# Performance work log

Hardware: AMD Instinct MI355X
Metric: run time of the kernel (lower is better)

## Reference

```python
import jax, jax.numpy as jnp
import numpy as np
import math

N_EMBD = 512
N_BRANCH = 4
BLOCK = 2048
B, T = 2, 2048


def make_rope_tables(dim, max_len):
    inv_freq = 1.0 / (10000.0 ** (np.arange(0, dim, 2, dtype=np.float32) / dim))
    t = np.arange(max_len, dtype=np.float32)
    freqs = np.einsum('i,j->ij', t, inv_freq)  # [max_len, dim/2]
    return jnp.asarray(np.cos(freqs)), jnp.asarray(np.sin(freqs))


def apply_rope(xq, cos, sin):
    # xq: [..., T, C]; cos/sin: [T, C/2]
    x1 = xq[..., 0::2]
    x2 = xq[..., 1::2]
    y1 = x1 * cos - x2 * sin
    y2 = x1 * sin + x2 * cos
    return jnp.stack((y1, y2), axis=-1).reshape(xq.shape)


def setup_inputs() -> dict:
    key = jax.random.key(0)
    ks = jax.random.split(key, 6)
    C, NB = N_EMBD, N_BRANCH
    s = 1.0 / math.sqrt(C)
    a = jax.random.normal(ks[0], (B, T, C), jnp.float32)
    x = jax.random.normal(ks[1], (B, T, C), jnp.float32)
    Wq = jax.random.normal(ks[2], (C, C * NB), jnp.float32) * s
    Wk = jax.random.normal(ks[3], (C, C), jnp.float32) * s
    Wv = jax.random.normal(ks[4], (C, C * NB), jnp.float32) * s
    Wo = jax.random.normal(ks[5], (C, C), jnp.float32) * s
    cos, sin = make_rope_tables(C, BLOCK)
    return {"a": a, "x": x, "Wq": Wq, "Wk": Wk, "Wv": Wv, "Wo": Wo,
            "cos": cos, "sin": sin}


def reference(a, x, Wq, Wk, Wv, Wo, cos, sin):
    Bb, Tt, C = x.shape
    NB = Wq.shape[1] // C
    cos_t = cos[:Tt]
    sin_t = sin[:Tt]

    q = (a @ Wq).reshape(Bb, Tt, NB, C).transpose(0, 2, 1, 3)  # [B,NB,T,C]
    v = (a @ Wv).reshape(Bb, Tt, NB, C).transpose(0, 2, 1, 3)  # [B,NB,T,C]
    k = (x @ Wk)[:, None, :, :]                                # [B,1,T,C]

    q = apply_rope(q, cos_t, sin_t)
    k = apply_rope(k, cos_t, sin_t)

    att = jnp.einsum('bntc,bosc->bnts', q, k) / math.sqrt(C)   # [B,NB,T,T]
    causal = jnp.tril(jnp.ones((Tt, Tt), bool))                # [T,T]
    att_m = jnp.where(causal, att, -jnp.inf)

    # softmax over branch axis; mask is identical across branches, so compute
    # on unmasked logits and zero-out masked positions (== nan_to_num of
    # softmax over fully -inf columns)
    soft_probs = jnp.where(causal, jax.nn.softmax(att, axis=1), 0.0)

    max_val = jnp.max(soft_probs, axis=1, keepdims=True)
    hard_mask = jax.lax.stop_gradient((soft_probs == max_val).astype(att.dtype))
    route_mask = jax.lax.stop_gradient(hard_mask - soft_probs) + soft_probs

    att_max = jnp.max(att_m, axis=1)                           # [B,T,T]
    attn_probs = jax.nn.softmax(att_max, axis=-1)              # [B,T,T]

    combined = attn_probs[:, None, :, :] * route_mask          # [B,NB,T,T]
    y = jnp.einsum('bnts,bnsc->btc', combined, v)              # [B,T,C]
    return y @ Wo
```

## Files before the change

kernel.cpp:

```cpp
#include <hip/hip_runtime.h>
#include <math.h>


#define B_ 2
#define T_ 2048
#define C_ 512
#define NB_ 4
#define C2_ 1024

typedef unsigned short u16;
typedef unsigned char u8;
using short8 = __attribute__((ext_vector_type(8))) short;
using bf16x8 = __attribute__((ext_vector_type(8))) __bf16;
using f32x4  = __attribute__((ext_vector_type(4))) float;

__device__ __forceinline__ float bf2f(u16 u) {
  union { unsigned int i; float f; } v; v.i = ((unsigned int)u) << 16; return v.f;
}
__device__ __forceinline__ u16 f2bf(float f) {
  union { float f; unsigned int i; } v; v.f = f;
  unsigned int u = v.i;
  return (u16)((u + 0x7fffu + ((u >> 16) & 1u)) >> 16);
}
__device__ __forceinline__ f32x4 mfma16x16x32(short8 a, short8 b, f32x4 c) {
  return __builtin_amdgcn_mfma_f32_16x16x32_bf16(
      __builtin_bit_cast(bf16x8, a), __builtin_bit_cast(bf16x8, b), c, 0, 0, 0);
}
__device__ __forceinline__ void split8(const float* s, uint4& hi, uint4& lo) {
  u16 h[8], l[8];
#pragma unroll
  for (int j = 0; j < 8; ++j) {
    h[j] = f2bf(s[j]);
    l[j] = f2bf(s[j] - bf2f(h[j]));
  }
  hi.x = h[0] | ((unsigned)h[1] << 16); hi.y = h[2] | ((unsigned)h[3] << 16);
  hi.z = h[4] | ((unsigned)h[5] << 16); hi.w = h[6] | ((unsigned)h[7] << 16);
  lo.x = l[0] | ((unsigned)l[1] << 16); lo.y = l[2] | ((unsigned)l[3] << 16);
  lo.z = l[4] | ((unsigned)l[5] << 16); lo.w = l[6] | ((unsigned)l[7] << 16);
}
__device__ __forceinline__ int swz(int row) { return ((row >> 1) & 3) << 3; }

template <int MODE>
__global__ __launch_bounds__(256) void gemm_qk(const float* __restrict__ A,
                                               const float* __restrict__ W,
                                               u16* __restrict__ out,
                                               const float* __restrict__ cosT,
                                               const float* __restrict__ sinT,
                                               const int N, const int K) {
  __shared__ u16 Ah[64][32], Al[64][32];
  __shared__ u16 Bh[64][32], Bl[64][32];
  const int tid = threadIdx.x;
  const int wave = tid >> 6, lane = tid & 63;
  const int m0 = blockIdx.y << 6, n0 = blockIdx.x << 6;
  const f32x4 zero = {0.f, 0.f, 0.f, 0.f};
  f32x4 acc[4] = {zero, zero, zero, zero};
  const int srow = tid >> 2, koff = ((tid & 3) << 3) ^ swz(tid >> 2);
  const int lrow = lane & 15, lk = ((lane >> 4) << 3) ^ swz(lane & 15);
  for (int kk = 0; kk < K; kk += 32) {
    const int kg = (tid & 3) << 3;
    float av[8];
    *(float4*)(av) = *(const float4*)(&A[(size_t)(m0 + srow) * K + kk + kg]);
    *(float4*)(av + 4) =
        *(const float4*)(&A[(size_t)(m0 + srow) * K + kk + kg + 4]);
    uint4 hi, lo;
    split8(av, hi, lo);
    *(uint4*)(&Ah[srow][koff]) = hi;
    *(uint4*)(&Al[srow][koff]) = lo;
    float wv[8];
#pragma unroll
    for (int j = 0; j < 8; ++j)
      wv[j] = W[(size_t)(kk + kg + j) * N + n0 + srow];
    split8(wv, hi, lo);
    *(uint4*)(&Bh[srow][koff]) = hi;
    *(uint4*)(&Bl[srow][koff]) = lo;
    __syncthreads();
    short8 ah = *(const short8*)(&Ah[(wave << 4) + lrow][lk]);
    short8 al = *(const short8*)(&Al[(wave << 4) + lrow][lk]);
#pragma unroll
    for (int ns = 0; ns < 4; ++ns) {
      short8 bh = *(const short8*)(&Bh[(ns << 4) + lrow][lk]);
      short8 bl = *(const short8*)(&Bl[(ns << 4) + lrow][lk]);
      acc[ns] = mfma16x16x32(ah, bh, acc[ns]);
      acc[ns] = mfma16x16x32(al, bh, acc[ns]);
      acc[ns] = mfma16x16x32(ah, bl, acc[ns]);
    }
    __syncthreads();
  }
  const int r0 = m0 + (wave << 4) + ((lane >> 4) << 2);
  const int cb = n0 + (lane & 15);
#pragma unroll
  for (int ns = 0; ns < 4; ++ns) {
#pragma unroll
    for (int r = 0; r < 4; ++r) {
      const int rg = r0 + r;
      const int cg = cb + (ns << 4);
      float v = acc[ns][r];
      float pv = __shfl_xor(v, 1);
      const int t = rg & (T_ - 1);
      const int c = (MODE == 1) ? (cg & (C_ - 1)) : cg;
      const int i = c >> 1;
      const float cf = cosT[(t << 8) + i];
      const float sf = sinT[(t << 8) + i];
      float x1 = (lane & 1) ? pv : v;
      float x2 = (lane & 1) ? v : pv;
      float y = (lane & 1) ? (x1 * sf + x2 * cf) : (x1 * cf - x2 * sf);
      if (MODE == 1) y *= 0.044194173824159216f;
      const u16 hi = f2bf(y);
      const u16 lo = f2bf(y - bf2f(hi));
      size_t rowoff;
      if (MODE == 1) {
        const int b = rg >> 11, n = cg >> 9;
        rowoff = ((size_t)((b * NB_ + n) * T_ + t)) * C2_;
      } else {
        rowoff = (size_t)rg * C2_;
      }
      out[rowoff + c] = hi;
      out[rowoff + C_ + c] = lo;
    }
  }
}

template <int AF32, int OF32>
__global__ __launch_bounds__(256) void gemm_hi(const void* __restrict__ Ap,
                                               const float* __restrict__ W,
                                               void* __restrict__ outp,
                                               const int N, const int K) {
  __shared__ u16 As[64][32];
  __shared__ u16 Bs[64][32];
  const int tid = threadIdx.x;
  const int wave = tid >> 6, lane = tid & 63;
  const int m0 = blockIdx.y << 6, n0 = blockIdx.x << 6;
  const f32x4 zero = {0.f, 0.f, 0.f, 0.f};
  f32x4 acc[4] = {zero, zero, zero, zero};
  const int srow = tid >> 2, koff = ((tid & 3) << 3) ^ swz(tid >> 2);
  const int lrow = lane & 15, lk = ((lane >> 4) << 3) ^ swz(lane & 15);
  for (int kk = 0; kk < K; kk += 32) {
    const int kg = (tid & 3) << 3;
    if (AF32) {
      const float* A = (const float*)Ap;
      float av[8];
      *(float4*)(av) = *(const float4*)(&A[(size_t)(m0 + srow) * K + kk + kg]);
      *(float4*)(av + 4) =
          *(const float4*)(&A[(size_t)(m0 + srow) * K + kk + kg + 4]);
      uint4 hi;
      hi.x = f2bf(av[0]) | ((unsigned)f2bf(av[1]) << 16);
      hi.y = f2bf(av[2]) | ((unsigned)f2bf(av[3]) << 16);
      hi.z = f2bf(av[4]) | ((unsigned)f2bf(av[5]) << 16);
      hi.w = f2bf(av[6]) | ((unsigned)f2bf(av[7]) << 16);
      *(uint4*)(&As[srow][koff]) = hi;
    } else {
      const u16* A = (const u16*)Ap;
      *(uint4*)(&As[srow][koff]) =
          *(const uint4*)(&A[(size_t)(m0 + srow) * K + kk + kg]);
    }
    uint4 hi;
    {
      float w[8];
#pragma unroll
      for (int j = 0; j < 8; ++j)
        w[j] = W[(size_t)(kk + kg + j) * N + n0 + srow];
      hi.x = f2bf(w[0]) | ((unsigned)f2bf(w[1]) << 16);
      hi.y = f2bf(w[2]) | ((unsigned)f2bf(w[3]) << 16);
      hi.z = f2bf(w[4]) | ((unsigned)f2bf(w[5]) << 16);
      hi.w = f2bf(w[6]) | ((unsigned)f2bf(w[7]) << 16);
    }
    *(uint4*)(&Bs[srow][koff]) = hi;
    __syncthreads();
    short8 af = *(const short8*)(&As[(wave << 4) + lrow][lk]);
#pragma unroll
    for (int ns = 0; ns < 4; ++ns) {
      short8 bf = *(const short8*)(&Bs[(ns << 4) + lrow][lk]);
      acc[ns] = mfma16x16x32(af, bf, acc[ns]);
    }
    __syncthreads();
  }
  const int r0 = m0 + (wave << 4) + ((lane >> 4) << 2);
  const int cb = n0 + (lane & 15);
#pragma unroll
  for (int ns = 0; ns < 4; ++ns) {
#pragma unroll
    for (int r = 0; r < 4; ++r) {
      const size_t idx = (size_t)(r0 + r) * N + cb + (ns << 4);
      if (OF32) ((float*)outp)[idx] = acc[ns][r];
      else ((u16*)outp)[idx] = f2bf(acc[ns][r]);
    }
  }
}

__global__ __launch_bounds__(256) void transpose_v_k(const u16* __restrict__ Vraw,
                                                     u16* __restrict__ VT) {
  const int bid = blockIdx.x;
  const int ct = bid & 7;
  const int ttile = (bid >> 3) & 31;
  const int n = (bid >> 8) & 3;
  const int b = bid >> 10;
  __shared__ u16 tile[64][68];
  const int tid = threadIdx.x;
  const int rr = tid >> 4;
  const int cc = (tid & 15) << 2;
  const int t0 = ttile << 6, c0 = ct << 6;
#pragma unroll
  for (int it = 0; it < 4; ++it) {
    const int r = (it << 4) + rr;
    *(ushort4*)(&tile[r][cc]) = *(const ushort4*)(
        &Vraw[((size_t)((b << 11) + t0 + r)) * (NB_ * C_) + n * C_ + c0 + cc]);
  }
  __syncthreads();
#pragma unroll
  for (int it = 0; it < 4; ++it) {
    const int c = (it << 4) + rr;
    ushort4 w;
    w.x = tile[cc + 0][c]; w.y = tile[cc + 1][c];
    w.z = tile[cc + 2][c]; w.w = tile[cc + 3][c];
    *(ushort4*)(&VT[((size_t)((b * NB_ + n) * C_ + c0 + c)) * T_ + t0 + cc]) = w;
  }
}

__global__ __launch_bounds__(256) void scores_k(const u16* __restrict__ Qcat,
                                                const u16* __restrict__ Kcat,
                                                u16* __restrict__ Mout,
                                                u8* __restrict__ Mask) {
  const int tri = ((blockIdx.x & 7) * 66) + (blockIdx.x >> 3);
  int tt = (int)((sqrtf(8.f * (float)tri + 1.f) - 1.f) * 0.5f);
  while ((tt + 1) * (tt + 2) / 2 <= tri) ++tt;
  while (tt * (tt + 1) / 2 > tri) --tt;
  const int ss = tri - tt * (tt + 1) / 2;
  const int b = blockIdx.y;
  __shared__ __align__(16) u16 Qh[NB_][64][32], Ql[NB_][64][32];
  __shared__ __align__(16) u16 Kh[64][32], Kl[64][32];
  const int tid = threadIdx.x;
  const int wave = tid >> 6, lane = tid & 63;
  const int t0 = tt << 6, s0 = ss << 6;
  const f32x4 zero = {0.f, 0.f, 0.f, 0.f};
  f32x4 acc[NB_][4];
  for (int n = 0; n < NB_; ++n)
    for (int j = 0; j < 4; ++j) acc[n][j] = zero;
  const int srow = tid >> 2, kg = (tid & 3) << 3;
  const int lrow = lane & 15, lk = (lane >> 4) << 3;
  const int wrow = wave << 4;
  const size_t qstride = (size_t)T_ * C2_;
  const size_t qbase = ((size_t)(b * NB_ * T_ + t0 + srow)) * C2_ + kg;
  const size_t kbase = ((size_t)((b << 11) + s0 + srow)) * C2_ + kg;

  for (int kk = 0; kk < C_; kk += 32) {
#pragma unroll
    for (int n = 0; n < NB_; ++n) {
      const size_t qb = qbase + (size_t)n * qstride + kk;
      __builtin_amdgcn_global_load_lds(
          (const __attribute__((address_space(1))) void*)&Qcat[qb],
          (__attribute__((address_space(3))) void*)&Qh[n][wrow][0], 16, 0, 0);
      __builtin_amdgcn_global_load_lds(
          (const __attribute__((address_space(1))) void*)&Qcat[qb + C_],
          (__attribute__((address_space(3))) void*)&Ql[n][wrow][0], 16, 0, 0);
    }
    __builtin_amdgcn_global_load_lds(
        (const __attribute__((address_space(1))) void*)&Kcat[kbase + kk],
        (__attribute__((address_space(3))) void*)&Kh[wrow][0], 16, 0, 0);
    __builtin_amdgcn_global_load_lds(
        (const __attribute__((address_space(1))) void*)&Kcat[kbase + kk + C_],
        (__attribute__((address_space(3))) void*)&Kl[wrow][0], 16, 0, 0);
    __syncthreads();
    short8 qh[NB_], ql[NB_];
#pragma unroll
    for (int n = 0; n < NB_; ++n) {
      qh[n] = *(const short8*)(&Qh[n][wrow + lrow][lk]);
      ql[n] = *(const short8*)(&Ql[n][wrow + lrow][lk]);
    }
#pragma unroll
    for (int ns = 0; ns < 4; ++ns) {
      short8 kh = *(const short8*)(&Kh[(ns << 4) + lrow][lk]);
      short8 kl = *(const short8*)(&Kl[(ns << 4) + lrow][lk]);
#pragma unroll
      for (int n = 0; n < NB_; ++n) {
        acc[n][ns] = mfma16x16x32(qh[n], kh, acc[n][ns]);
        acc[n][ns] = mfma16x16x32(ql[n], kh, acc[n][ns]);
        acc[n][ns] = mfma16x16x32(qh[n], kl, acc[n][ns]);
      }
    }
    __syncthreads();
  }
  const int tb = t0 + (wave << 4) + ((lane >> 4) << 2);
  const int sb = s0 + (lane & 15);
#pragma unroll
  for (int ns = 0; ns < 4; ++ns) {
#pragma unroll
    for (int r = 0; r < 4; ++r) {
      const int t = tb + r, s = sb + (ns << 4);
      float a0 = acc[0][ns][r], a1 = acc[1][ns][r];
      float a2 = acc[2][ns][r], a3 = acc[3][ns][r];
      float m = fmaxf(fmaxf(a0, a1), fmaxf(a2, a3));
      u8 msk = (u8)((a0 == m) | ((a1 == m) << 1) | ((a2 == m) << 2) |
                    ((a3 == m) << 3));
      if (s > t) { m = -__builtin_inff(); msk = 0; }
      const size_t idx = (size_t)b * T_ * T_ + (size_t)t * T_ + s;
      Mout[idx] = f2bf(m);
      Mask[idx] = msk;
    }
  }
}

__global__ __launch_bounds__(256) void rowstats_k(const u16* __restrict__ Mb,
                                                  float* __restrict__ Rm,
                                                  float* __restrict__ Rz) {
  const int r = (blockIdx.x << 2) + (threadIdx.x >> 6);
  const int lane = threadIdx.x & 63;
  const int b = r >> 11, t = r & (T_ - 1);
  const u16* row = Mb + (size_t)b * T_ * T_ + (size_t)t * T_;
  float m = -__builtin_inff();
  for (int s = lane; s <= t; s += 64) m = fmaxf(m, bf2f(row[s]));
#pragma unroll
  for (int off = 32; off; off >>= 1) m = fmaxf(m, __shfl_xor(m, off));
  float z = 0.f;
  for (int s = lane; s <= t; s += 64) z += __expf(bf2f(row[s]) - m);
#pragma unroll
  for (int off = 32; off; off >>= 1) z += __shfl_xor(z, off);
  if (lane == 0) { Rm[r] = m; Rz[r] = 1.f / z; }
}

__global__ __launch_bounds__(512) void pv_k(const u16* __restrict__ Mb,
                                            const float* __restrict__ Rm,
                                            const float* __restrict__ Rz,
                                            const u8* __restrict__ Mask,
                                            const u16* __restrict__ VT,
                                            u16* __restrict__ Y) {
  const int cblk = blockIdx.x, ypair = blockIdx.y, b = blockIdx.z;
  const int c0 = cblk << 6;
  __shared__ u16 Ps[NB_][64][32];
  __shared__ u16 Vs[NB_][64][32];
  const int tid = threadIdx.x;
  const int wave = tid >> 6, lane = tid & 63;
  const int wq = wave & 3, ch = wave >> 2;
  const int row8 = tid >> 3, off4 = (tid & 7) << 2;
  const int scol = off4 ^ swz(row8);
  const int lrow = lane & 15, lk = ((lane >> 4) << 3) ^ swz(lane & 15);
  const f32x4 zero = {0.f, 0.f, 0.f, 0.f};
  const size_t vrow_base[NB_] = {
      ((size_t)((b * NB_ + 0) * C_ + c0 + row8)) * T_,
      ((size_t)((b * NB_ + 1) * C_ + c0 + row8)) * T_,
      ((size_t)((b * NB_ + 2) * C_ + c0 + row8)) * T_,
      ((size_t)((b * NB_ + 3) * C_ + c0 + row8)) * T_};

  for (int half = 0; half < 2; ++half) {
    const int tt = half ? (31 - ypair) : ypair;
    const int t0 = tt << 6;
    const int nchunk = (tt + 1) << 1;
    const int rg = (b << 11) + t0 + row8;
    const size_t pro = (size_t)rg << 11;
    const float rm = Rm[rg], rz = Rz[rg];
    f32x4 acc[2] = {zero, zero};
    uint2 puA, puB; unsigned mkA, mkB; uint2 vvA[NB_], vvB[NB_];

    puA = *(const uint2*)(&Mb[pro + off4]);
    mkA = *(const unsigned*)(&Mask[pro + off4]);
#pragma unroll
    for (int n = 0; n < NB_; ++n)
      vvA[n] = *(const uint2*)(&VT[vrow_base[n] + off4]);
    puB = *(const uint2*)(&Mb[pro + 32 + off4]);
    mkB = *(const unsigned*)(&Mask[pro + 32 + off4]);
#pragma unroll
    for (int n = 0; n < NB_; ++n)
      vvB[n] = *(const uint2*)(&VT[vrow_base[n] + 32 + off4]);

    for (int ck = 0; ck < nchunk; ck += 2) {
      {
        u16 m4[4] = {(u16)puA.x, (u16)(puA.x >> 16), (u16)puA.y,
                     (u16)(puA.y >> 16)};
        u16 p[4];
#pragma unroll
        for (int j = 0; j < 4; ++j)
          p[j] = f2bf(__expf(bf2f(m4[j]) - rm) * rz);
        u8 mk[4] = {(u8)mkA, (u8)(mkA >> 8), (u8)(mkA >> 16), (u8)(mkA >> 24)};
#pragma unroll
        for (int n = 0; n < NB_; ++n) {
          uint2 wv;
          wv.x = (unsigned)(((mk[0] >> n) & 1) ? p[0] : 0) |
                 ((unsigned)(((mk[1] >> n) & 1) ? p[1] : 0) << 16);
          wv.y = (unsigned)(((mk[2] >> n) & 1) ? p[2] : 0) |
                 ((unsigned)(((mk[3] >> n) & 1) ? p[3] : 0) << 16);
          *(uint2*)(&Ps[n][row8][scol]) = wv;
          *(uint2*)(&Vs[n][row8][scol]) = vvA[n];
        }
        if (ck + 2 < nchunk) {
          const int sB = (ck + 2) << 5;
          puA = *(const uint2*)(&Mb[pro + sB + off4]);
          mkA = *(const unsigned*)(&Mask[pro + sB + off4]);
#pragma unroll
          for (int n = 0; n < NB_; ++n)
            vvA[n] = *(const uint2*)(&VT[vrow_base[n] + sB + off4]);
        }
        __syncthreads();
#pragma unroll
        for (int n = 0; n < NB_; ++n) {
          short8 af = *(const short8*)(&Ps[n][(wq << 4) + lrow][lk]);
#pragma unroll
          for (int cs = 0; cs < 2; ++cs) {
            short8 bf =
                *(const short8*)(&Vs[n][(ch << 5) + (cs << 4) + lrow][lk]);
            acc[cs] = mfma16x16x32(af, bf, acc[cs]);
          }
        }
        __syncthreads();
      }
      {
        u16 m4[4] = {(u16)puB.x, (u16)(puB.x >> 16), (u16)puB.y,
                     (u16)(puB.y >> 16)};
        u16 p[4];
#pragma unroll
        for (int j = 0; j < 4; ++j)
          p[j] = f2bf(__expf(bf2f(m4[j]) - rm) * rz);
        u8 mk[4] = {(u8)mkB, (u8)(mkB >> 8), (u8)(mkB >> 16), (u8)(mkB >> 24)};
#pragma unroll
        for (int n = 0; n < NB_; ++n) {
          uint2 wv;
          wv.x = (unsigned)(((mk[0] >> n) & 1) ? p[0] : 0) |
                 ((unsigned)(((mk[1] >> n) & 1) ? p[1] : 0) << 16);
          wv.y = (unsigned)(((mk[2] >> n) & 1) ? p[2] : 0) |
                 ((unsigned)(((mk[3] >> n) & 1) ? p[3] : 0) << 16);
          *(uint2*)(&Ps[n][row8][scol]) = wv;
          *(uint2*)(&Vs[n][row8][scol]) = vvB[n];
        }
        if (ck + 3 < nchunk) {
          const int sB = (ck + 3) << 5;
          puB = *(const uint2*)(&Mb[pro + sB + off4]);
          mkB = *(const unsigned*)(&Mask[pro + sB + off4]);
#pragma unroll
          for (int n = 0; n < NB_; ++n)
            vvB[n] = *(const uint2*)(&VT[vrow_base[n] + sB + off4]);
        }
        __syncthreads();
#pragma unroll
        for (int n = 0; n < NB_; ++n) {
          short8 af = *(const short8*)(&Ps[n][(wq << 4) + lrow][lk]);
#pragma unroll
          for (int cs = 0; cs < 2; ++cs) {
            short8 bf =
                *(const short8*)(&Vs[n][(ch << 5) + (cs << 4) + lrow][lk]);
            acc[cs] = mfma16x16x32(af, bf, acc[cs]);
          }
        }
        __syncthreads();
      }
    }
    const int tb = t0 + (wq << 4) + ((lane >> 4) << 2);
    const int cbs = c0 + (ch << 5) + (lane & 15);
#pragma unroll
    for (int cs = 0; cs < 2; ++cs) {
#pragma unroll
      for (int r = 0; r < 4; ++r) {
        Y[(size_t)((b << 11) + tb + r) * C_ + cbs + (cs << 4)] =
            f2bf(acc[cs][r]);
      }
    }
  }
}

extern "C" void kernel_launch(void* const* d_in, const int* in_sizes, int n_in,
                              void* d_out, int out_size, void* d_ws,
                              size_t ws_size, hipStream_t stream) {
  (void)in_sizes; (void)n_in; (void)out_size; (void)ws_size;
  const float* a    = (const float*)d_in[0];
  const float* x    = (const float*)d_in[1];
  const float* Wq   = (const float*)d_in[2];
  const float* Wk   = (const float*)d_in[3];
  const float* Wv   = (const float*)d_in[4];
  const float* Wo   = (const float*)d_in[5];
  const float* cosT = (const float*)d_in[6];
  const float* sinT = (const float*)d_in[7];

  char* w = (char*)d_ws;
  u16* Qcat   = (u16*)(w + 0);
  u16* Kcat   = (u16*)(w + 33554432);
  u16* Vraw   = (u16*)(w + 41943040);
  u16* VT     = (u16*)(w + 58720256);
  u8*  Mask   = (u8*)(w + 75497472);
  float* Rm   = (float*)(w + 83886080);
  float* Rz   = (float*)(w + 83902464);
  u16* Mb     = Vraw;
  u16* Y      = Qcat;

  const dim3 blk(256);
  gemm_qk<1><<<dim3(32, 64), blk, 0, stream>>>(a, Wq, Qcat, cosT, sinT, 2048, 512);
  gemm_qk<2><<<dim3(8, 64), blk, 0, stream>>>(x, Wk, Kcat, cosT, sinT, 512, 512);
  gemm_hi<1, 0><<<dim3(32, 64), blk, 0, stream>>>(a, Wv, (void*)Vraw, 2048, 512);
  transpose_v_k<<<dim3(2048), blk, 0, stream>>>(Vraw, VT);
  scores_k<<<dim3(528, 2), blk, 0, stream>>>(Qcat, Kcat, Mb, Mask);
  rowstats_k<<<dim3(1024), blk, 0, stream>>>(Mb, Rm, Rz);
  pv_k<<<dim3(8, 16, 2), dim3(512), 0, stream>>>(Mb, Rm, Rz, Mask, VT, Y);
  gemm_hi<0, 1><<<dim3(8, 64), blk, 0, stream>>>(Y, Wo, d_out, 512, 512);
}
```

Baseline: 344.8 us.

## Pre-split inputs and weights to bf16 hi/lo once, use direct-to-LDS GEMMs

Adds pre-pass kernels that convert the activation `a` into concatenated bf16 hi/lo planes and transpose-split Wq and Wv into bf16 layouts once. The Q and V projection GEMMs are replaced with kernels that read these pre-split operands through global_load_lds straight into shared memory. This removes the repeated fp32-to-bf16 splitting each GEMM tile did on every reload and cuts global read traffic. In exchange it adds three extra launches and workspace traffic. The new GEMMs drop the LDS swizzle, so shared-memory bank conflicts may appear.

New measurement: 317.0 us, median of 2. -8.1%, faster.

```diff
diff --git a/kernel.cpp b/kernel.cpp
--- a/kernel.cpp
+++ b/kernel.cpp
@@ -39,6 +39,166 @@
   lo.z = l[4] | ((unsigned)l[5] << 16); lo.w = l[6] | ((unsigned)l[7] << 16);
 }
 __device__ __forceinline__ int swz(int row) { return ((row >> 1) & 3) << 3; }
+
+__global__ __launch_bounds__(256) void split_a_k(const float* __restrict__ A,
+                                                 u16* __restrict__ Acat) {
+  const size_t base = ((size_t)blockIdx.x * 256 + threadIdx.x) << 3;
+  const size_t row = base >> 9, col = base & 511;
+  float av[8];
+  *(float4*)(av) = *(const float4*)(&A[base]);
+  *(float4*)(av + 4) = *(const float4*)(&A[base + 4]);
+  uint4 hi, lo;
+  split8(av, hi, lo);
+  *(uint4*)(&Acat[row * C2_ + col]) = hi;
+  *(uint4*)(&Acat[row * C2_ + C_ + col]) = lo;
+}
+
+template <int HILO>
+__global__ __launch_bounds__(256) void splitT_w_k(const float* __restrict__ W,
+                                                  u16* __restrict__ WT,
+                                                  const int N) {
+  __shared__ float tile[64][68];
+  const int n0 = blockIdx.x << 6, k0 = blockIdx.y << 6;
+  const int tid = threadIdx.x;
+  const int rr = tid >> 4, cc = (tid & 15) << 2;
+#pragma unroll
+  for (int it = 0; it < 4; ++it) {
+    const int kr = (it << 4) + rr;
+    *(float4*)(&tile[kr][cc]) =
+        *(const float4*)(&W[(size_t)(k0 + kr) * N + n0 + cc]);
+  }
+  __syncthreads();
+  const int W2 = HILO ? C2_ : C_;
+#pragma unroll
+  for (int it = 0; it < 4; ++it) {
+    const int nr = (it << 4) + rr;
+    const int kc = cc;
+    float v[4] = {tile[kc][nr], tile[kc + 1][nr], tile[kc + 2][nr],
+                  tile[kc + 3][nr]};
+    ushort4 hw, lw;
+    hw.x = f2bf(v[0]); hw.y = f2bf(v[1]); hw.z = f2bf(v[2]); hw.w = f2bf(v[3]);
+    *(ushort4*)(&WT[(size_t)(n0 + nr) * W2 + k0 + kc]) = hw;
+    if (HILO) {
+      lw.x = f2bf(v[0] - bf2f(hw.x)); lw.y = f2bf(v[1] - bf2f(hw.y));
+      lw.z = f2bf(v[2] - bf2f(hw.z)); lw.w = f2bf(v[3] - bf2f(hw.w));
+      *(ushort4*)(&WT[(size_t)(n0 + nr) * W2 + C_ + k0 + kc]) = lw;
+    }
+  }
+}
+
+__global__ __launch_bounds__(256) void gemm_qk_pre(const u16* __restrict__ Acat,
+                                                   const u16* __restrict__ WT,
+                                                   u16* __restrict__ out,
+                                                   const float* __restrict__ cosT,
+                                                   const float* __restrict__ sinT) {
+  __shared__ __align__(16) u16 Ah[64][32], Al[64][32];
+  __shared__ __align__(16) u16 Bh[64][32], Bl[64][32];
+  const int tid = threadIdx.x;
+  const int wave = tid >> 6, lane = tid & 63;
+  const int m0 = blockIdx.y << 6, n0 = blockIdx.x << 6;
+  const f32x4 zero = {0.f, 0.f, 0.f, 0.f};
+  f32x4 acc[4] = {zero, zero, zero, zero};
+  const int srow = tid >> 2, kg = (tid & 3) << 3;
+  const int lrow = lane & 15, lk = (lane >> 4) << 3;
+  const int wrow = wave << 4;
+  const size_t abase = (size_t)(m0 + srow) * C2_ + kg;
+  const size_t bbase = (size_t)(n0 + srow) * C2_ + kg;
+  for (int kk = 0; kk < C_; kk += 32) {
+    __builtin_amdgcn_global_load_lds(
+        (const __attribute__((address_space(1))) void*)&Acat[abase + kk],
+        (__attribute__((address_space(3))) void*)&Ah[wrow][0], 16, 0, 0);
+    __builtin_amdgcn_global_load_lds(
+        (const __attribute__((address_space(1))) void*)&Acat[abase + C_ + kk],
+        (__attribute__((address_space(3))) void*)&Al[wrow][0], 16, 0, 0);
+    __builtin_amdgcn_global_load_lds(
+        (const __attribute__((address_space(1))) void*)&WT[bbase + kk],
+        (__attribute__((address_space(3))) void*)&Bh[wrow][0], 16, 0, 0);
+    __builtin_amdgcn_global_load_lds(
+        (const __attribute__((address_space(1))) void*)&WT[bbase + C_ + kk],
+        (__attribute__((address_space(3))) void*)&Bl[wrow][0], 16, 0, 0);
+    __syncthreads();
+    short8 ah = *(const short8*)(&Ah[(wave << 4) + lrow][lk]);
+    short8 al = *(const short8*)(&Al[(wave << 4) + lrow][lk]);
+#pragma unroll
+    for (int ns = 0; ns < 4; ++ns) {
+      short8 bh = *(const short8*)(&Bh[(ns << 4) + lrow][lk]);
+      short8 bl = *(const short8*)(&Bl[(ns << 4) + lrow][lk]);
+      acc[ns] = mfma16x16x32(ah, bh, acc[ns]);
+      acc[ns] = mfma16x16x32(al, bh, acc[ns]);
+      acc[ns] = mfma16x16x32(ah, bl, acc[ns]);
+    }
+    __syncthreads();
+  }
+  const int r0 = m0 + (wave << 4) + ((lane >> 4) << 2);
+  const int cb = n0 + (lane & 15);
+#pragma unroll
+  for (int ns = 0; ns < 4; ++ns) {
+#pragma unroll
+    for (int r = 0; r < 4; ++r) {
+      const int rg = r0 + r;
+      const int cg = cb + (ns << 4);
+      float v = acc[ns][r];
+      float pv = __shfl_xor(v, 1);
+      const int t = rg & (T_ - 1);
+      const int c = cg & (C_ - 1);
+      const int i = c >> 1;
+      const float cf = cosT[(t << 8) + i];
+      const float sf = sinT[(t << 8) + i];
+      float x1 = (lane & 1) ? pv : v;
+      float x2 = (lane & 1) ? v : pv;
+      float y = (lane & 1) ? (x1 * sf + x2 * cf) : (x1 * cf - x2 * sf);
+      y *= 0.044194173824159216f;
+      const u16 hi = f2bf(y);
+      const u16 lo = f2bf(y - bf2f(hi));
+      const int b = rg >> 11, n = cg >> 9;
+      const size_t rowoff = ((size_t)((b * NB_ + n) * T_ + t)) * C2_;
+      out[rowoff + c] = hi;
+      out[rowoff + C_ + c] = lo;
+    }
+  }
+}
+
+__global__ __launch_bounds__(256) void gemm_bb(const u16* __restrict__ Acat,
+                                               const u16* __restrict__ WT,
+                                               u16* __restrict__ out) {
+  __shared__ __align__(16) u16 As[64][32];
+  __shared__ __align__(16) u16 Bs[64][32];
+  const int tid = threadIdx.x;
+  const int wave = tid >> 6, lane = tid & 63;
+  const int m0 = blockIdx.y << 6, n0 = blockIdx.x << 6;
+  const f32x4 zero = {0.f, 0.f, 0.f, 0.f};
+  f32x4 acc[4] = {zero, zero, zero, zero};
+  const int srow = tid >> 2, kg = (tid & 3) << 3;
+  const int lrow = lane & 15, lk = (lane >> 4) << 3;
+  const int wrow = wave << 4;
+  const size_t abase = (size_t)(m0 + srow) * C2_ + kg;
+  const size_t bbase = (size_t)(n0 + srow) * C_ + kg;
+  for (int kk = 0; kk < C_; kk += 32) {
+    __builtin_amdgcn_global_load_lds(
+        (const __attribute__((address_space(1))) void*)&Acat[abase + kk],
+        (__attribute__((address_space(3))) void*)&As[wrow][0], 16, 0, 0);
+    __builtin_amdgcn_global_load_lds(
+        (const __attribute__((address_space(1))) void*)&WT[bbase + kk],
+        (__attribute__((address_space(3))) void*)&Bs[wrow][0], 16, 0, 0);
+    __syncthreads();
+    short8 af = *(const short8*)(&As[(wave << 4) + lrow][lk]);
+#pragma unroll
+    for (int ns = 0; ns < 4; ++ns) {
+      short8 bf = *(const short8*)(&Bs[(ns << 4) + lrow][lk]);
+      acc[ns] = mfma16x16x32(af, bf, acc[ns]);
+    }
+    __syncthreads();
+  }
+  const int r0 = m0 + (wave << 4) + ((lane >> 4) << 2);
+  const int cb = n0 + (lane & 15);
+#pragma unroll
+  for (int ns = 0; ns < 4; ++ns) {
+#pragma unroll
+    for (int r = 0; r < 4; ++r) {
+      out[(size_t)(r0 + r) * (NB_ * C_) + cb + (ns << 4)] = f2bf(acc[ns][r]);
+    }
+  }
+}
 
 template <int MODE>
 __global__ __launch_bounds__(256) void gemm_qk(const float* __restrict__ A,
@@ -475,13 +635,19 @@
   u8*  Mask   = (u8*)(w + 75497472);
   float* Rm   = (float*)(w + 83886080);
   float* Rz   = (float*)(w + 83902464);
+  u16* Acat   = (u16*)(w + 83918848);
+  u16* WTq    = (u16*)(w + 92307456);
+  u16* WTv    = (u16*)(w + 96501760);
   u16* Mb     = Vraw;
   u16* Y      = Qcat;
 
   const dim3 blk(256);
-  gemm_qk<1><<<dim3(32, 64), blk, 0, stream>>>(a, Wq, Qcat, cosT, sinT, 2048, 512);
+  split_a_k<<<dim3(1024), blk, 0, stream>>>(a, Acat);
+  splitT_w_k<1><<<dim3(32, 8), blk, 0, stream>>>(Wq, WTq, 2048);
+  splitT_w_k<0><<<dim3(32, 8), blk, 0, stream>>>(Wv, WTv, 2048);
+  gemm_qk_pre<<<dim3(32, 64), blk, 0, stream>>>(Acat, WTq, Qcat, cosT, sinT);
   gemm_qk<2><<<dim3(8, 64), blk, 0, stream>>>(x, Wk, Kcat, cosT, sinT, 512, 512);
-  gemm_hi<1, 0><<<dim3(32, 64), blk, 0, stream>>>(a, Wv, (void*)Vraw, 2048, 512);
+  gemm_bb<<<dim3(32, 64), blk, 0, stream>>>(Acat, WTv, Vraw);
   transpose_v_k<<<dim3(2048), blk, 0, stream>>>(Vraw, VT);
   scores_k<<<dim3(528, 2), blk, 0, stream>>>(Qcat, Kcat, Mb, Mask);
   rowstats_k<<<dim3(1024), blk, 0, stream>>>(Mb, Rm, Rz);
```
